# Kernel optimization log

Hardware: AMD Instinct MI355X
Metric: run time of the kernel (lower is better)

The kernel has to match this reference:

```python
import jax, jax.numpy as jnp
import numpy as np

B = 8192
D_IN = 1024    # rb_encoder_input_siz
D_CTRL = 64    # rb_control_siz
D_STATE = 1024 # rb_state_siz
H = 2048       # mlp_hidden_sizes / decoder_hidden_sizes


def _linear_init(key, fan_in, fan_out):
    # torch.nn.Linear default init: U(-1/sqrt(fan_in), 1/sqrt(fan_in))
    kw, kb = jax.random.split(key)
    bound = 1.0 / np.sqrt(fan_in)
    W = jax.random.uniform(kw, (fan_in, fan_out), jnp.float32, -bound, bound)
    b = jax.random.uniform(kb, (fan_out,), jnp.float32, -bound, bound)
    return W, b


def setup_inputs() -> dict:
    key = jax.random.key(0)
    ks = jax.random.split(key, 7)
    x = jax.random.normal(ks[0], (B, D_IN), jnp.float32)
    We1, be1 = _linear_init(ks[1], D_IN, H)
    We2, be2 = _linear_init(ks[2], H, H)
    We3, be3 = _linear_init(ks[3], H, D_CTRL)
    Wd1, bd1 = _linear_init(ks[4], D_CTRL, H)
    Wd2, bd2 = _linear_init(ks[5], H, H)
    Wd3, bd3 = _linear_init(ks[6], H, D_STATE)
    return {"x": x,
            "We1": We1, "be1": be1, "We2": We2, "be2": be2, "We3": We3, "be3": be3,
            "Wd1": Wd1, "bd1": bd1, "Wd2": Wd2, "bd2": bd2, "Wd3": Wd3, "bd3": bd3}


def _mlp3(x, W1, b1, W2, b2, W3, b3):
    h = jax.nn.relu(x @ W1 + b1)
    h = jax.nn.relu(h @ W2 + b2)
    return h @ W3 + b3


def rb_to_ratio(x):
    # squash raw control logits to (0,1) ratios
    return jax.nn.sigmoid(x)


def reference(x, We1, be1, We2, be2, We3, be3, Wd1, bd1, Wd2, bd2, Wd3, bd3):
    x = x.reshape(x.shape[0], -1)
    control_vec = rb_to_ratio(_mlp3(x, We1, be1, We2, be2, We3, be3))  # [B, 64]
    state_vec = _mlp3(control_vec, Wd1, bd1, Wd2, bd2, Wd3, bd3)       # [B, 1024]
    return (control_vec, state_vec)
```

## Files before the change

kernel.cpp:

```cpp
#include <hip/hip_runtime.h>
#include <hip/hip_bf16.h>
#include <cstdint>
#include <cstddef>


typedef __bf16 bf16_t;
typedef bf16_t bf16x8 __attribute__((ext_vector_type(8)));
typedef bf16_t bf16x4 __attribute__((ext_vector_type(4)));
typedef float  floatx4 __attribute__((ext_vector_type(4)));

__device__ __forceinline__ void async_cp16(const bf16_t* gp, bf16_t* lp) {
    __builtin_amdgcn_global_load_lds(
        (const __attribute__((address_space(1))) void*)gp,
        (__attribute__((address_space(3))) void*)lp, 16, 0, 0);
}

struct PrepArgs {
    const float* x; bf16_t* xb;
    const float* w[6]; bf16_t* t[6];
};

__device__ __forceinline__ void trans_tile(const float* __restrict__ in,
                                           bf16_t* __restrict__ out,
                                           int K, int N, int bx, int by,
                                           int tx, int ty,
                                           float (*tile)[33]) {
    const int n0 = bx * 32, k0 = by * 32;
#pragma unroll
    for (int i = 0; i < 32; i += 8)
        tile[ty + i][tx] = in[(size_t)(k0 + ty + i) * N + n0 + tx];
    __syncthreads();
#pragma unroll
    for (int i = 0; i < 32; i += 8)
        out[(size_t)(n0 + ty + i) * K + k0 + tx] = (bf16_t)tile[tx][ty + i];
}

__global__ __launch_bounds__(256) void prep(PrepArgs a) {
    __shared__ float tile[32][33];
    const int tx = threadIdx.x, ty = threadIdx.y;
    const int b = blockIdx.x;
    if (b < 8192) {
        const int i = (b * 256 + ty * 32 + tx) * 4;
        const float4 v = *(const float4*)(a.x + i);
        bf16x4 o;
        o[0] = (bf16_t)v.x; o[1] = (bf16_t)v.y;
        o[2] = (bf16_t)v.z; o[3] = (bf16_t)v.w;
        *(bf16x4*)(a.xb + i) = o;
        return;
    }
    int lb = b - 8192;
    if (lb < 2048)      { trans_tile(a.w[0], a.t[0], 1024, 2048, lb % 64, lb / 64, tx, ty, tile); return; }
    lb -= 2048;
    if (lb < 4096)      { trans_tile(a.w[1], a.t[1], 2048, 2048, lb % 64, lb / 64, tx, ty, tile); return; }
    lb -= 4096;
    if (lb < 128)       { trans_tile(a.w[2], a.t[2], 2048, 64,   lb % 2,  lb / 2,  tx, ty, tile); return; }
    lb -= 128;
    if (lb < 128)       { trans_tile(a.w[3], a.t[3], 64,   2048, lb % 64, lb / 64, tx, ty, tile); return; }
    lb -= 128;
    if (lb < 4096)      { trans_tile(a.w[4], a.t[4], 2048, 2048, lb % 64, lb / 64, tx, ty, tile); return; }
    lb -= 4096;
    trans_tile(a.w[5], a.t[5], 2048, 1024, lb % 32, lb / 32, tx, ty, tile);
}

__global__ __launch_bounds__(512, 2)
void gemm256(const bf16_t* __restrict__ A, const bf16_t* __restrict__ Bt,
             const float* __restrict__ bias, bf16_t* __restrict__ C,
             int N, int K, int ld) {
    constexpr int TSZ  = 256 * 64;
    constexpr int BUFS = 2 * TSZ;
    __shared__ __align__(16) bf16_t sm[2 * BUFS];

    const int tid  = threadIdx.x;
    const int lane = tid & 63;
    const int wave = __builtin_amdgcn_readfirstlane(tid >> 6);
    const int wm = wave >> 2, wn = wave & 3;

    const int lin = blockIdx.x;
    const int xcd = lin & 7, loc = lin >> 3;
    const int m0 = (xcd * 4 + (loc >> 3)) * 256;
    const int n0 = (loc & 7) * 256;

    const int lrow = lane >> 3, lch = lane & 7;
    const int sw   = (lch ^ lrow) * 8;
    const bf16_t* Acom = A  + (size_t)(m0 + lrow) * ld + sw;
    const bf16_t* Bcom = Bt + (size_t)(n0 + lrow) * ld + sw;
    int aS[4], bS[4];
    aS[0] = wave;     aS[1] = wave + 16;
    aS[2] = wave + 8; aS[3] = wave + 24;
    const int bb = (wave >> 1) * 8 + (wave & 1) * 2;
    bS[0] = bb;     bS[1] = bb + 1;
    bS[2] = bb + 4; bS[3] = bb + 5;
    const bf16_t* aP[4]; const bf16_t* bP[4];
    int aLo[4], bLo[4];
#pragma unroll
    for (int i = 0; i < 4; ++i) {
        aP[i] = Acom + (size_t)aS[i] * 8 * ld;  aLo[i] = aS[i] * 512;
        bP[i] = Bcom + (size_t)bS[i] * 8 * ld;  bLo[i] = bS[i] * 512;
    }

    const int r15 = lane & 15, kg = lane >> 4;
    const int xk0 = ( kg      ^ lch) * 8;
    const int xk1 = ((kg + 4) ^ lch) * 8;
    const int aB0 = (wm * 128 + r15) * 64 + xk0;
    const int aB1 = (wm * 128 + r15) * 64 + xk1;
    const int bB0 = (wn * 64  + r15) * 64 + xk0;
    const int bB1 = (wn * 64  + r15) * 64 + xk1;

    floatx4 acc[8][4];
#pragma unroll
    for (int i = 0; i < 8; ++i)
#pragma unroll
        for (int j = 0; j < 4; ++j) acc[i][j] = floatx4{0.f, 0.f, 0.f, 0.f};

    const int nKT = K >> 6;

    async_cp16(aP[0], sm + aLo[0]);
    async_cp16(aP[1], sm + aLo[1]);
    async_cp16(bP[0], sm + TSZ + bLo[0]);
    async_cp16(bP[1], sm + TSZ + bLo[1]);
    async_cp16(aP[2], sm + aLo[2]);
    async_cp16(aP[3], sm + aLo[3]);
    async_cp16(bP[2], sm + TSZ + bLo[2]);
    async_cp16(bP[3], sm + TSZ + bLo[3]);

#define G256_READ_A(DST, MU) \
    _Pragma("unroll") \
    for (int f = 0; f < 4; ++f) { \
        DST[f][0] = *(const bf16x8*)(bufA + (MU) * 4096 + f * 1024 + aB0); \
        DST[f][1] = *(const bf16x8*)(bufA + (MU) * 4096 + f * 1024 + aB1); \
    }

#define G256_READ_B(DST, NU) \
    _Pragma("unroll") \
    for (int g = 0; g < 2; ++g) { \
        DST[g][0] = *(const bf16x8*)(bufB + (NU) * 2048 + g * 1024 + bB0); \
        DST[g][1] = *(const bf16x8*)(bufB + (NU) * 2048 + g * 1024 + bB1); \
    }

#define G256_MFMA(AF, BF, I0, J0) \
    __builtin_amdgcn_s_setprio(1); \
    _Pragma("unroll") \
    for (int f = 0; f < 4; ++f) \
    _Pragma("unroll") \
    for (int g = 0; g < 2; ++g) { \
        acc[(I0) + f][(J0) + g] = __builtin_amdgcn_mfma_f32_16x16x32_bf16( \
            AF[f][0], BF[g][0], acc[(I0) + f][(J0) + g], 0, 0, 0); \
        acc[(I0) + f][(J0) + g] = __builtin_amdgcn_mfma_f32_16x16x32_bf16( \
            AF[f][1], BF[g][1], acc[(I0) + f][(J0) + g], 0, 0, 0); \
    } \
    __builtin_amdgcn_s_setprio(0);

    bf16x8 af0[4][2], af1[4][2], bfg0[2][2], bfg1[2][2];
    for (int t = 0; t < nKT; ++t) {
        const bf16_t* bufA = sm + (t & 1) * BUFS;
        const bf16_t* bufB = bufA + TSZ;
        bf16_t* nA = sm + ((t + 1) & 1) * BUFS;
        bf16_t* nB = nA + TSZ;
        const int tn = (t + 1 == nKT) ? 0 : t + 1;
        const size_t ko = (size_t)tn * 64;

        asm volatile("s_waitcnt vmcnt(0)" ::: "memory");
        __builtin_amdgcn_s_barrier();
        __builtin_amdgcn_sched_barrier(0);

        G256_READ_A(af0, 0);
        G256_READ_B(bfg0, 0);
        G256_READ_A(af1, 1);
        G256_READ_B(bfg1, 1);

        async_cp16(aP[0] + ko, nA + aLo[0]);
        async_cp16(aP[1] + ko, nA + aLo[1]);
        async_cp16(bP[0] + ko, nB + bLo[0]);
        async_cp16(bP[1] + ko, nB + bLo[1]);
        async_cp16(aP[2] + ko, nA + aLo[2]);
        async_cp16(aP[3] + ko, nA + aLo[3]);
        async_cp16(bP[2] + ko, nB + bLo[2]);
        async_cp16(bP[3] + ko, nB + bLo[3]);

        G256_MFMA(af0, bfg0, 0, 0);
        G256_MFMA(af1, bfg0, 4, 0);
        G256_MFMA(af1, bfg1, 4, 2);
        G256_MFMA(af0, bfg1, 0, 2);
    }

    asm volatile("s_waitcnt vmcnt(0)" ::: "memory");

#undef G256_READ_A
#undef G256_READ_B
#undef G256_MFMA

    const int row_l = kg * 4;
#pragma unroll
    for (int j = 0; j < 4; ++j) {
        const int n = n0 + wn * 64 + j * 16 + r15;
        const float bv = bias[n];
#pragma unroll
        for (int i = 0; i < 8; ++i) {
            const int m = m0 + wm * 128 + i * 16 + row_l;
#pragma unroll
            for (int r = 0; r < 4; ++r) {
                float f = acc[i][j][r] + bv;
                f = fmaxf(f, 0.f);
                C[(size_t)(m + r) * N + n] = (bf16_t)f;
            }
        }
    }
}

template<int BM, int BN, int WM, int WN, int ACT, int OMODE, int GX>
__global__ __launch_bounds__(256)
void gemm_bt(const bf16_t* __restrict__ A, const bf16_t* __restrict__ Bt,
             const float* __restrict__ bias,
             bf16_t* __restrict__ Cb, float* __restrict__ Cf,
             int M, int N, int K, int ld) {
    constexpr int BK = 32;
    constexpr int MI = WM / 16, NI = WN / 16;
    constexpr int WCOLS = BN / WN;
    static_assert((BM / WM) * (BN / WN) == 4, "4 waves");
    constexpr int A_CPW = (BM * BK) / (8 * 64 * 4);
    constexpr int B_CPW = (BN * BK) / (8 * 64 * 4);
    static_assert(A_CPW >= 1 && B_CPW >= 1, "tile too small");
    constexpr int ASZ = BM * BK, BSZ = BN * BK;

    __shared__ bf16_t As[2 * ASZ];
    __shared__ bf16_t Bs[2 * BSZ];

    const int lin = blockIdx.x;
    const int xcd = lin & 7;
    const int loc = lin >> 3;
    const int by  = xcd * 8 + loc / GX;
    const int bx  = loc % GX;

    const int tid  = threadIdx.x;
    const int wave = tid >> 6;
    const int lane = tid & 63;
    const int m0 = by * BM;
    const int n0 = bx * BN;
    const int kz0 = blockIdx.y * K;
    const int wm0 = (wave / WCOLS) * WM;
    const int wn0 = (wave % WCOLS) * WN;
    const int r15 = lane & 15;
    const int kgc = lane >> 4;

    floatx4 acc[MI][NI];
#pragma unroll
    for (int i = 0; i < MI; ++i)
#pragma unroll
        for (int j = 0; j < NI; ++j)
            acc[i][j] = floatx4{0.f, 0.f, 0.f, 0.f};

    const bf16_t* a_src[A_CPW];
    int a_dst[A_CPW];
#pragma unroll
    for (int i = 0; i < A_CPW; ++i) {
        const int cbase = (wave * A_CPW + i) * 64;
        const int chunk = cbase + lane;
        const int row = chunk >> 2;
        const int c8  = (((chunk & 3) - (row >> 1)) & 3) * 8;
        a_src[i] = A + (size_t)(m0 + row) * ld + kz0 + c8;
        a_dst[i] = cbase * 8;
    }
    const bf16_t* b_src[B_CPW];
    int b_dst[B_CPW];
#pragma unroll
    for (int i = 0; i < B_CPW; ++i) {
        const int cbase = (wave * B_CPW + i) * 64;
        const int chunk = cbase + lane;
        const int row = chunk >> 2;
        const int c8  = (((chunk & 3) - (row >> 1)) & 3) * 8;
        b_src[i] = Bt + (size_t)(n0 + row) * ld + kz0 + c8;
        b_dst[i] = cbase * 8;
    }
    int a_off[MI], b_off[NI];
#pragma unroll
    for (int i = 0; i < MI; ++i) {
        const int r = wm0 + i * 16 + r15;
        a_off[i] = r * BK + (((kgc + (r >> 1)) & 3) << 3);
    }
#pragma unroll
    for (int j = 0; j < NI; ++j) {
        const int r = wn0 + j * 16 + r15;
        b_off[j] = r * BK + (((kgc + (r >> 1)) & 3) << 3);
    }

    const int nIter = K / BK;
#pragma unroll
    for (int i = 0; i < A_CPW; ++i) async_cp16(a_src[i], As + a_dst[i]);
#pragma unroll
    for (int i = 0; i < B_CPW; ++i) async_cp16(b_src[i], Bs + b_dst[i]);

    for (int it = 0; it < nIter; ++it) {
        __syncthreads();
        if (it + 1 < nIter) {
            const int kn = (it + 1) * BK;
            const int nb = (it + 1) & 1;
#pragma unroll
            for (int i = 0; i < A_CPW; ++i)
                async_cp16(a_src[i] + kn, As + nb * ASZ + a_dst[i]);
#pragma unroll
            for (int i = 0; i < B_CPW; ++i)
                async_cp16(b_src[i] + kn, Bs + nb * BSZ + b_dst[i]);
        }
        const bf16_t* curA = As + (it & 1) * ASZ;
        const bf16_t* curB = Bs + (it & 1) * BSZ;

        bf16x8 af[MI], bfr[NI];
#pragma unroll
        for (int i = 0; i < MI; ++i)
            af[i] = *(const bf16x8*)(curA + a_off[i]);
#pragma unroll
        for (int j = 0; j < NI; ++j)
            bfr[j] = *(const bf16x8*)(curB + b_off[j]);
#pragma unroll
        for (int i = 0; i < MI; ++i)
#pragma unroll
            for (int j = 0; j < NI; ++j)
                acc[i][j] = __builtin_amdgcn_mfma_f32_16x16x32_bf16(
                    af[i], bfr[j], acc[i][j], 0, 0, 0);
    }

    const int row_l = (lane >> 4) * 4;
#pragma unroll
    for (int j = 0; j < NI; ++j) {
        const int n = n0 + wn0 + j * 16 + r15;
        const float bv = (OMODE & 4) ? 0.f : bias[n];
#pragma unroll
        for (int i = 0; i < MI; ++i) {
            const int m = m0 + wm0 + i * 16 + row_l;
#pragma unroll
            for (int r = 0; r < 4; ++r) {
                float f = acc[i][j][r] + bv;
                if (ACT == 1) f = fmaxf(f, 0.f);
                if (ACT == 2) f = 1.f / (1.f + __expf(-f));
                const size_t idx = (size_t)(m + r) * N + n;
                if (OMODE & 1) Cb[idx] = (bf16_t)f;
                if (OMODE & 2) Cf[idx] = f;
                if (OMODE & 4) Cf[(size_t)blockIdx.y * ((size_t)M * N) + idx] = f;
            }
        }
    }
}

__global__ __launch_bounds__(256)
void e3_reduce(const float* __restrict__ part, const float* __restrict__ be3,
               float* __restrict__ out0, bf16_t* __restrict__ cb) {
    const int t = blockIdx.x * 256 + threadIdx.x;
    const size_t P = (size_t)8192 * 64;
    float s = part[t] + part[t + P] + part[t + 2 * P] + part[t + 3 * P]
            + be3[t & 63];
    const float f = 1.f / (1.f + __expf(-s));
    out0[t] = f;
    cb[t] = (bf16_t)f;
}

extern "C" void kernel_launch(void* const* d_in, const int* in_sizes, int n_in,
                              void* d_out, int out_size, void* d_ws, size_t ws_size,
                              hipStream_t stream) {
    const float* x   = (const float*)d_in[0];
    const float* We1 = (const float*)d_in[1];
    const float* be1 = (const float*)d_in[2];
    const float* We2 = (const float*)d_in[3];
    const float* be2 = (const float*)d_in[4];
    const float* We3 = (const float*)d_in[5];
    const float* be3 = (const float*)d_in[6];
    const float* Wd1 = (const float*)d_in[7];
    const float* bd1 = (const float*)d_in[8];
    const float* Wd2 = (const float*)d_in[9];
    const float* bd2 = (const float*)d_in[10];
    const float* Wd3 = (const float*)d_in[11];
    const float* bd3 = (const float*)d_in[12];

    char* ws = (char*)d_ws;
    size_t off = 0;
    bf16_t* xb  = (bf16_t*)(ws + off); off += (size_t)8192 * 1024 * 2;
    bf16_t* w1t = (bf16_t*)(ws + off); off += (size_t)2048 * 1024 * 2;
    bf16_t* w2t = (bf16_t*)(ws + off); off += (size_t)2048 * 2048 * 2;
    bf16_t* w3t = (bf16_t*)(ws + off); off += (size_t)64   * 2048 * 2;
    bf16_t* w4t = (bf16_t*)(ws + off); off += (size_t)2048 * 64   * 2;
    bf16_t* w5t = (bf16_t*)(ws + off); off += (size_t)2048 * 2048 * 2;
    bf16_t* w6t = (bf16_t*)(ws + off); off += (size_t)1024 * 2048 * 2;
    bf16_t* ha  = (bf16_t*)(ws + off); off += (size_t)8192 * 2048 * 2;
    bf16_t* hb  = (bf16_t*)(ws + off); off += (size_t)8192 * 2048 * 2;
    bf16_t* cb  = (bf16_t*)(ws + off); off += (size_t)8192 * 64   * 2;
    float* e3part = (float*)ha;

    float* out0 = (float*)d_out;
    float* out1 = out0 + (size_t)8192 * 64;

    PrepArgs pa;
    pa.x = x; pa.xb = xb;
    pa.w[0] = We1; pa.w[1] = We2; pa.w[2] = We3;
    pa.w[3] = Wd1; pa.w[4] = Wd2; pa.w[5] = Wd3;
    pa.t[0] = w1t; pa.t[1] = w2t; pa.t[2] = w3t;
    pa.t[3] = w4t; pa.t[4] = w5t; pa.t[5] = w6t;
    prep<<<dim3(20736), dim3(32, 8), 0, stream>>>(pa);

    gemm256<<<dim3(256), dim3(512), 0, stream>>>(xb, w1t, be1, ha, 2048, 1024, 1024);
    gemm256<<<dim3(256), dim3(512), 0, stream>>>(ha, w2t, be2, hb, 2048, 2048, 2048);
    gemm_bt<128, 64, 32, 64, 0, 4, 1><<<dim3(64, 4), 256, 0, stream>>>(
        hb, w3t, nullptr, nullptr, e3part, 8192, 64, 512, 2048);
    e3_reduce<<<dim3(2048), 256, 0, stream>>>(e3part, be3, out0, cb);
    gemm_bt<128, 128, 64, 64, 1, 1, 16><<<dim3(16 * 64), 256, 0, stream>>>(
        cb, w4t, bd1, ha, nullptr, 8192, 2048, 64, 64);
    gemm256<<<dim3(256), dim3(512), 0, stream>>>(ha, w5t, bd2, hb, 2048, 2048, 2048);
    gemm_bt<128, 128, 64, 64, 0, 2, 8><<<dim3(8 * 64), 256, 0, stream>>>(
        hb, w6t, bd3, nullptr, out1, 8192, 1024, 2048, 2048);
}
```

Baseline: 366.3 us.

## Software-pipeline GEMM main loop interleaving LDS fragment reads with MFMA

Restructures the double-buffered GEMM K-loop into a two-iteration unrolled body. It issues the next tile's async global-to-LDS copies first, then interleaves LDS fragment reads with MFMA groups under sched_barriers. After the wait and barrier, it preloads the first A/B fragments of the next tile, so LDS read latency overlaps with MFMA work instead of stalling before it. The cost is extra register pressure from duplicate fragment sets. The 2x unroll also assumes an even number of K tiles.

Result: slower. 568.1 us (+55.1%).

```diff
diff --git a/kernel.cpp b/kernel.cpp
--- a/kernel.cpp
+++ b/kernel.cpp
@@ -114,27 +114,18 @@
 
     const int nKT = K >> 6;
 
-    async_cp16(aP[0], sm + aLo[0]);
-    async_cp16(aP[1], sm + aLo[1]);
-    async_cp16(bP[0], sm + TSZ + bLo[0]);
-    async_cp16(bP[1], sm + TSZ + bLo[1]);
-    async_cp16(aP[2], sm + aLo[2]);
-    async_cp16(aP[3], sm + aLo[3]);
-    async_cp16(bP[2], sm + TSZ + bLo[2]);
-    async_cp16(bP[3], sm + TSZ + bLo[3]);
-
-#define G256_READ_A(DST, MU) \
+#define G256_RD_A(DST, BUF, MU) \
     _Pragma("unroll") \
     for (int f = 0; f < 4; ++f) { \
-        DST[f][0] = *(const bf16x8*)(bufA + (MU) * 4096 + f * 1024 + aB0); \
-        DST[f][1] = *(const bf16x8*)(bufA + (MU) * 4096 + f * 1024 + aB1); \
-    }
-
-#define G256_READ_B(DST, NU) \
+        DST[f][0] = *(const bf16x8*)((BUF) + (MU) * 4096 + f * 1024 + aB0); \
+        DST[f][1] = *(const bf16x8*)((BUF) + (MU) * 4096 + f * 1024 + aB1); \
+    }
+
+#define G256_RD_B(DST, BUF, NU) \
     _Pragma("unroll") \
     for (int g = 0; g < 2; ++g) { \
-        DST[g][0] = *(const bf16x8*)(bufB + (NU) * 2048 + g * 1024 + bB0); \
-        DST[g][1] = *(const bf16x8*)(bufB + (NU) * 2048 + g * 1024 + bB1); \
+        DST[g][0] = *(const bf16x8*)((BUF) + (NU) * 2048 + g * 1024 + bB0); \
+        DST[g][1] = *(const bf16x8*)((BUF) + (NU) * 2048 + g * 1024 + bB1); \
     }
 
 #define G256_MFMA(AF, BF, I0, J0) \
@@ -150,43 +141,65 @@
     } \
     __builtin_amdgcn_s_setprio(0);
 
-    bf16x8 af0[4][2], af1[4][2], bfg0[2][2], bfg1[2][2];
-    for (int t = 0; t < nKT; ++t) {
-        const bf16_t* bufA = sm + (t & 1) * BUFS;
-        const bf16_t* bufB = bufA + TSZ;
-        bf16_t* nA = sm + ((t + 1) & 1) * BUFS;
-        bf16_t* nB = nA + TSZ;
-        const int tn = (t + 1 == nKT) ? 0 : t + 1;
-        const size_t ko = (size_t)tn * 64;
-
-        asm volatile("s_waitcnt vmcnt(0)" ::: "memory");
-        __builtin_amdgcn_s_barrier();
-        __builtin_amdgcn_sched_barrier(0);
-
-        G256_READ_A(af0, 0);
-        G256_READ_B(bfg0, 0);
-        G256_READ_A(af1, 1);
-        G256_READ_B(bfg1, 1);
-
-        async_cp16(aP[0] + ko, nA + aLo[0]);
-        async_cp16(aP[1] + ko, nA + aLo[1]);
-        async_cp16(bP[0] + ko, nB + bLo[0]);
-        async_cp16(bP[1] + ko, nB + bLo[1]);
-        async_cp16(aP[2] + ko, nA + aLo[2]);
-        async_cp16(aP[3] + ko, nA + aLo[3]);
-        async_cp16(bP[2] + ko, nB + bLo[2]);
-        async_cp16(bP[3] + ko, nB + bLo[3]);
-
-        G256_MFMA(af0, bfg0, 0, 0);
-        G256_MFMA(af1, bfg0, 4, 0);
-        G256_MFMA(af1, bfg1, 4, 2);
-        G256_MFMA(af0, bfg1, 0, 2);
-    }
-
+#define G256_BODY(CA, CB, NXA, NXB, T, P) do { \
+    const bf16_t* bufA = sm + (P) * BUFS; \
+    const bf16_t* bufB = bufA + TSZ; \
+    bf16_t* nA = sm + (1 - (P)) * BUFS; \
+    bf16_t* nB = nA + TSZ; \
+    const int tn = ((T) + 1 == nKT) ? 0 : (T) + 1; \
+    const size_t ko = (size_t)tn * 64; \
+    async_cp16(aP[0] + ko, nA + aLo[0]); \
+    async_cp16(aP[1] + ko, nA + aLo[1]); \
+    async_cp16(aP[2] + ko, nA + aLo[2]); \
+    async_cp16(aP[3] + ko, nA + aLo[3]); \
+    async_cp16(bP[0] + ko, nB + bLo[0]); \
+    async_cp16(bP[1] + ko, nB + bLo[1]); \
+    async_cp16(bP[2] + ko, nB + bLo[2]); \
+    async_cp16(bP[3] + ko, nB + bLo[3]); \
+    __builtin_amdgcn_sched_barrier(0); \
+    G256_RD_A(af1, bufA, 1); \
+    G256_MFMA(CA, CB, 0, 0); \
+    __builtin_amdgcn_sched_barrier(0); \
+    G256_RD_B(bfg1, bufB, 1); \
+    G256_MFMA(af1, CB, 4, 0); \
+    __builtin_amdgcn_sched_barrier(0); \
+    asm volatile("s_waitcnt vmcnt(0)" ::: "memory"); \
+    __builtin_amdgcn_s_barrier(); \
+    __builtin_amdgcn_sched_barrier(0); \
+    G256_RD_A(NXA, nA, 0); \
+    G256_MFMA(af1, bfg1, 4, 2); \
+    __builtin_amdgcn_sched_barrier(0); \
+    G256_RD_B(NXB, nB, 0); \
+    G256_MFMA(CA, bfg1, 0, 2); \
+    __builtin_amdgcn_sched_barrier(0); \
+} while (0)
+
+    bf16x8 af0A[4][2], af0B[4][2], bf0A[2][2], bf0B[2][2];
+    bf16x8 af1[4][2], bfg1[2][2];
+
+    async_cp16(aP[0], sm + aLo[0]);
+    async_cp16(aP[1], sm + aLo[1]);
+    async_cp16(aP[2], sm + aLo[2]);
+    async_cp16(aP[3], sm + aLo[3]);
+    async_cp16(bP[0], sm + TSZ + bLo[0]);
+    async_cp16(bP[1], sm + TSZ + bLo[1]);
+    async_cp16(bP[2], sm + TSZ + bLo[2]);
+    async_cp16(bP[3], sm + TSZ + bLo[3]);
     asm volatile("s_waitcnt vmcnt(0)" ::: "memory");
-
-#undef G256_READ_A
-#undef G256_READ_B
+    __builtin_amdgcn_s_barrier();
+    G256_RD_A(af0A, sm, 0);
+    G256_RD_B(bf0A, sm + TSZ, 0);
+
+    for (int t = 0; t < nKT; t += 2) {
+        G256_BODY(af0A, bf0A, af0B, bf0B, t,     0);
+        G256_BODY(af0B, bf0B, af0A, bf0A, t + 1, 1);
+    }
+
+    asm volatile("s_waitcnt vmcnt(0)" ::: "memory");
+
+#undef G256_BODY
+#undef G256_RD_A
+#undef G256_RD_B
 #undef G256_MFMA
 
     const int row_l = kg * 4;
```
